# Optimization experiments

Measured on AMD Instinct MI355X. Metric: run time of the kernel, lower is better.

The kernel has to match this reference:

```python
import jax, jax.numpy as jnp
import numpy as np

MAX_DISP = 64


def setup_inputs() -> dict:
    key = jax.random.key(0)
    k1, k2 = jax.random.split(key)
    b, c, h, w = 4, 256, 180, 320
    left_feature = jax.random.normal(k1, (b, c, h, w), dtype=jnp.float32)
    right_feature = jax.random.normal(k2, (b, c, h, w), dtype=jnp.float32)
    return {"left_feature": left_feature, "right_feature": right_feature}


def reference(left_feature, right_feature):
    # Correlation cost volume: cost[:, i, :, x] = mean_c(left[:, :, :, x] * right[:, :, :, x - i])
    # for x >= i, else 0. Loop is over the small fixed disparity range (init arg).
    b, c, h, w = left_feature.shape
    slices = []
    for i in range(MAX_DISP):
        if i > 0:
            prod = jnp.mean(left_feature[:, :, :, i:] * right_feature[:, :, :, :-i], axis=1)  # [b, h, w-i]
            prod = jnp.pad(prod, ((0, 0), (0, 0), (i, 0)))  # zero-fill columns < i
        else:
            prod = jnp.mean(left_feature * right_feature, axis=1)  # [b, h, w]
        slices.append(prod)
    cost_volume = jnp.stack(slices, axis=1)  # [b, max_disp, h, w]
    return cost_volume
```

## Files before the change

### kernel.cpp

```cpp
#include <hip/hip_runtime.h>


typedef short bf16x8 __attribute__((ext_vector_type(8)));
typedef float f32x4 __attribute__((ext_vector_type(4)));

#define Bb 4
#define Cc 256
#define Hh 180
#define Ww 320
#define MAXD 64
#define KC 32
#define NCHUNK (Cc / KC)
#define RSTR 20
#define HW (Hh * Ww)

__device__ __forceinline__ unsigned int bf16rne2(float a, float b) {
    unsigned int ua = __float_as_uint(a);
    unsigned int ub = __float_as_uint(b);
    ua = (ua + 0x7FFFu + ((ua >> 16) & 1u)) >> 16;
    ub = (ub + 0x7FFFu + ((ub >> 16) & 1u)) & 0xFFFF0000u;
    return ua | ub;
}

__global__ __launch_bounds__(320, 3)
void _AA_CostVolume_63668595196248_kernel(const float* __restrict__ L,
                                          const float* __restrict__ R,
                                          float* __restrict__ out) {
    __shared__ unsigned int sL[Ww * RSTR];
    __shared__ unsigned int sR[Ww * RSTR];

    const int tid = threadIdx.x;
    const int bi  = blockIdx.x;
    const int b   = bi / Hh;
    const int h   = bi % Hh;

    {
        const int ob = (b * MAXD * Hh + h) * Ww;
        for (int z = tid; z < MAXD * MAXD; z += 320) {
            const int i = z >> 6;
            const int x = z & 63;
            if (x < i) out[ob + i * HW + x] = 0.0f;
        }
    }

    const int lane = tid & 63;
    const int w    = tid >> 6;
    const int q    = lane >> 4;
    const int n    = lane & 15;

    const int cp = tid & 15;
    const int tq = tid >> 4;
    const int inbase = (b * Cc + 2 * cp) * HW + h * Ww;

    const int frag_off = n * RSTR + 4 * q;

    f32x4 acc[4][5];
#pragma unroll
    for (int xt = 0; xt < 4; ++xt)
#pragma unroll
        for (int du = 0; du < 5; ++du) {
            f32x4 z = {0.f, 0.f, 0.f, 0.f};
            acc[xt][du] = z;
        }

    for (int kc = 0; kc < NCHUNK; ++kc) {
        __syncthreads();
        const float* Lp = L + inbase + kc * KC * HW;
        const float* Rp = R + inbase + kc * KC * HW;
#pragma unroll
        for (int s = 0; s < 4; ++s) {
            const int xq = tq + 20 * s;
            const float4 l0 = *(const float4*)(Lp + 4 * xq);
            const float4 l1 = *(const float4*)(Lp + HW + 4 * xq);
            const float4 r0 = *(const float4*)(Rp + 4 * xq);
            const float4 r1 = *(const float4*)(Rp + HW + 4 * xq);
            const float* l0f = (const float*)&l0;
            const float* l1f = (const float*)&l1;
            const float* r0f = (const float*)&r0;
            const float* r1f = (const float*)&r1;
#pragma unroll
            for (int j = 0; j < 4; ++j) {
                sL[(4 * xq + j) * RSTR + cp] = bf16rne2(l0f[j], l1f[j]);
                sR[(4 * xq + j) * RSTR + cp] = bf16rne2(r0f[j], r1f[j]);
            }
        }
        __syncthreads();

        bf16x8 af[4];
#pragma unroll
        for (int xt = 0; xt < 4; ++xt)
            af[xt] = *(const bf16x8*)&sL[(16 * (4 * w + xt) + n) * RSTR + 4 * q];

#pragma unroll
        for (int uu = 0; uu < 8; ++uu) {
            const int u = 4 * w + uu - 4;
            if (u >= 0) {
                const bf16x8 bfr = *(const bf16x8*)&sR[u * (16 * RSTR) + frag_off];
#pragma unroll
                for (int xt = 0; xt < 4; ++xt) {
                    const int du = xt - (uu - 4);
                    if (du >= 0 && du <= 4)
                        acc[xt][du] = __builtin_amdgcn_mfma_f32_16x16x32_bf16(
                            af[xt], bfr, acc[xt][du], 0, 0, 0);
                }
            }
        }
    }

    const float sc = 1.0f / 256.0f;
#pragma unroll
    for (int xt = 0; xt < 4; ++xt) {
        const int t  = 4 * w + xt;
        const int x0 = 16 * t + 4 * q;
#pragma unroll
        for (int du = 0; du < 5; ++du) {
            if (t - du >= 0) {
                const int ib = 16 * du + 4 * q - n;
#pragma unroll
                for (int r = 0; r < 4; ++r) {
                    const int i = ib + r;
                    if (i >= 0 && i < MAXD)
                        out[((b * MAXD + i) * Hh + h) * Ww + x0 + r] = acc[xt][du][r] * sc;
                }
            }
        }
    }
}

extern "C" void kernel_launch(void* const* d_in, const int* in_sizes, int n_in,
                              void* d_out, int out_size, void* d_ws, size_t ws_size,
                              hipStream_t stream) {
    const float* left  = (const float*)d_in[0];
    const float* right = (const float*)d_in[1];
    float* out = (float*)d_out;
    dim3 grid(Bb * Hh);
    dim3 block(320);
    _AA_CostVolume_63668595196248_kernel<<<grid, block, 0, stream>>>(left, right, out);
}
```

Baseline: 501.8 us.

## Split rows into column halves and prefetch next channel chunk into registers

```diff
diff --git a/kernel.cpp b/kernel.cpp
--- a/kernel.cpp
+++ b/kernel.cpp
@@ -13,6 +13,8 @@
 #define NCHUNK (Cc / KC)
 #define RSTR 20
 #define HW (Hh * Ww)
+#define LROWS 160
+#define RROWS 224
 
 __device__ __forceinline__ unsigned int bf16rne2(float a, float b) {
     unsigned int ua = __float_as_uint(a);
@@ -22,19 +24,22 @@
     return ua | ub;
 }
 
-__global__ __launch_bounds__(320, 3)
+__global__ __launch_bounds__(320, 4)
 void _AA_CostVolume_63668595196248_kernel(const float* __restrict__ L,
                                           const float* __restrict__ R,
                                           float* __restrict__ out) {
-    __shared__ unsigned int sL[Ww * RSTR];
-    __shared__ unsigned int sR[Ww * RSTR];
+    __shared__ unsigned int sL[LROWS * RSTR];
+    __shared__ unsigned int sR[RROWS * RSTR];
 
     const int tid = threadIdx.x;
     const int bi  = blockIdx.x;
-    const int b   = bi / Hh;
-    const int h   = bi % Hh;
+    const int xh  = bi & 1;
+    const int rid = bi >> 1;
+    const int b   = rid / Hh;
+    const int h   = rid % Hh;
+    const int X0  = xh * 160;
 
-    {
+    if (xh == 0) {
         const int ob = (b * MAXD * Hh + h) * Ww;
         for (int z = tid; z < MAXD * MAXD; z += 320) {
             const int i = z >> 6;
@@ -50,71 +55,93 @@
 
     const int cp = tid & 15;
     const int tq = tid >> 4;
-    const int inbase = (b * Cc + 2 * cp) * HW + h * Ww;
+
+    const float* baseL = L + (b * Cc + 2 * cp) * HW + h * Ww + X0;
+    const float* baseR = R + (b * Cc + 2 * cp) * HW + h * Ww + X0 - 64;
+
+    const bool rv0 = (xh != 0) || (tq >= 16);
+    const bool rv2 = (tq < 16);
 
     const int frag_off = n * RSTR + 4 * q;
+    const int luMin = (xh == 0) ? 4 : 0;
 
-    f32x4 acc[4][5];
+    f32x4 acc[2][5];
 #pragma unroll
-    for (int xt = 0; xt < 4; ++xt)
+    for (int xt = 0; xt < 2; ++xt)
 #pragma unroll
         for (int du = 0; du < 5; ++du) {
             f32x4 z = {0.f, 0.f, 0.f, 0.f};
             acc[xt][du] = z;
         }
 
+    float4 pl0a, pl0b, pl1a, pl1b;
+    float4 pr0a, pr0b, pr1a, pr1b, pr2a, pr2b;
+
+#define LOADCHUNK(KCI) do {                                               \
+        const int ko = (KCI) * (KC * HW);                                 \
+        pl0a = *(const float4*)(baseL + ko + 4 * tq);                     \
+        pl0b = *(const float4*)(baseL + ko + HW + 4 * tq);                \
+        pl1a = *(const float4*)(baseL + ko + 4 * (tq + 20));              \
+        pl1b = *(const float4*)(baseL + ko + HW + 4 * (tq + 20));         \
+        if (rv0) {                                                       \
+            pr0a = *(const float4*)(baseR + ko + 4 * tq);                 \
+            pr0b = *(const float4*)(baseR + ko + HW + 4 * tq);            \
+        }                                                                \
+        pr1a = *(const float4*)(baseR + ko + 4 * (tq + 20));              \
+        pr1b = *(const float4*)(baseR + ko + HW + 4 * (tq + 20));         \
+        if (rv2) {                                                       \
+            pr2a = *(const float4*)(baseR + ko + 4 * (tq + 40));          \
+            pr2b = *(const float4*)(baseR + ko + HW + 4 * (tq + 40));     \
+        }                                                                \
+    } while (0)
+
+#define STORE4(SBUF, ROW0, VA, VB) do {                                   \
+        const float* _fa = (const float*)&(VA);                           \
+        const float* _fb = (const float*)&(VB);                           \
+        _Pragma("unroll")                                                 \
+        for (int j = 0; j < 4; ++j)                                       \
+            SBUF[((ROW0) + j) * RSTR + cp] = bf16rne2(_fa[j], _fb[j]);    \
+    } while (0)
+
+    LOADCHUNK(0);
+
     for (int kc = 0; kc < NCHUNK; ++kc) {
         __syncthreads();
-        const float* Lp = L + inbase + kc * KC * HW;
-        const float* Rp = R + inbase + kc * KC * HW;
-#pragma unroll
-        for (int s = 0; s < 4; ++s) {
-            const int xq = tq + 20 * s;
-            const float4 l0 = *(const float4*)(Lp + 4 * xq);
-            const float4 l1 = *(const float4*)(Lp + HW + 4 * xq);
-            const float4 r0 = *(const float4*)(Rp + 4 * xq);
-            const float4 r1 = *(const float4*)(Rp + HW + 4 * xq);
-            const float* l0f = (const float*)&l0;
-            const float* l1f = (const float*)&l1;
-            const float* r0f = (const float*)&r0;
-            const float* r1f = (const float*)&r1;
-#pragma unroll
-            for (int j = 0; j < 4; ++j) {
-                sL[(4 * xq + j) * RSTR + cp] = bf16rne2(l0f[j], l1f[j]);
-                sR[(4 * xq + j) * RSTR + cp] = bf16rne2(r0f[j], r1f[j]);
-            }
-        }
+        STORE4(sL, 4 * tq, pl0a, pl0b);
+        STORE4(sL, 4 * (tq + 20), pl1a, pl1b);
+        if (rv0) STORE4(sR, 4 * tq, pr0a, pr0b);
+        STORE4(sR, 4 * (tq + 20), pr1a, pr1b);
+        if (rv2) STORE4(sR, 4 * (tq + 40), pr2a, pr2b);
         __syncthreads();
 
-        bf16x8 af[4];
-#pragma unroll
-        for (int xt = 0; xt < 4; ++xt)
-            af[xt] = *(const bf16x8*)&sL[(16 * (4 * w + xt) + n) * RSTR + 4 * q];
+        if (kc + 1 < NCHUNK) LOADCHUNK(kc + 1);
+
+        const bf16x8 af0 = *(const bf16x8*)&sL[(16 * (2 * w + 0) + n) * RSTR + 4 * q];
+        const bf16x8 af1 = *(const bf16x8*)&sL[(16 * (2 * w + 1) + n) * RSTR + 4 * q];
 
 #pragma unroll
-        for (int uu = 0; uu < 8; ++uu) {
-            const int u = 4 * w + uu - 4;
-            if (u >= 0) {
-                const bf16x8 bfr = *(const bf16x8*)&sR[u * (16 * RSTR) + frag_off];
-#pragma unroll
-                for (int xt = 0; xt < 4; ++xt) {
-                    const int du = xt - (uu - 4);
-                    if (du >= 0 && du <= 4)
-                        acc[xt][du] = __builtin_amdgcn_mfma_f32_16x16x32_bf16(
-                            af[xt], bfr, acc[xt][du], 0, 0, 0);
-                }
+        for (int uu = 0; uu < 6; ++uu) {
+            const int lu = 2 * w + uu;
+            if (lu >= luMin) {
+                const bf16x8 bfr = *(const bf16x8*)&sR[lu * (16 * RSTR) + frag_off];
+                if (uu <= 4)
+                    acc[0][4 - uu] = __builtin_amdgcn_mfma_f32_16x16x32_bf16(
+                        af0, bfr, acc[0][4 - uu], 0, 0, 0);
+                if (uu >= 1)
+                    acc[1][5 - uu] = __builtin_amdgcn_mfma_f32_16x16x32_bf16(
+                        af1, bfr, acc[1][5 - uu], 0, 0, 0);
             }
         }
     }
 
     const float sc = 1.0f / 256.0f;
 #pragma unroll
-    for (int xt = 0; xt < 4; ++xt) {
-        const int t  = 4 * w + xt;
-        const int x0 = 16 * t + 4 * q;
+    for (int xt = 0; xt < 2; ++xt) {
+        const int gt = 10 * xh + 2 * w + xt;
+        const int x0 = 16 * gt + 4 * q;
 #pragma unroll
         for (int du = 0; du < 5; ++du) {
-            if (t - du >= 0) {
+            if (gt - du >= 0) {
                 const int ib = 16 * du + 4 * q - n;
 #pragma unroll
                 for (int r = 0; r < 4; ++r) {
@@ -125,6 +152,8 @@
             }
         }
     }
+#undef LOADCHUNK
+#undef STORE4
 }
 
 extern "C" void kernel_launch(void* const* d_in, const int* in_sizes, int n_in,
@@ -133,7 +162,7 @@
     const float* left  = (const float*)d_in[0];
     const float* right = (const float*)d_in[1];
     float* out = (float*)d_out;
-    dim3 grid(Bb * Hh);
+    dim3 grid(2 * Bb * Hh);
     dim3 block(320);
     _AA_CostVolume_63668595196248_kernel<<<grid, block, 0, stream>>>(left, right, out);
 }
```

After: 508.0 us. No clear change (+1.2%).
